# Kernel optimization log

Measured on AMD Instinct MI355X. Metric: run time of the kernel, lower is better.

## Reference

```python
import jax, jax.numpy as jnp
import numpy as np

N_NODES = 40000
N_EDGES = 640000
D_IN = 128
D_OUT = 128


def setup_inputs() -> dict:
    key = jax.random.key(0)
    k1, k2, k3, k4, k5 = jax.random.split(key, 5)
    x = jax.random.normal(k1, (N_NODES, D_IN), dtype=jnp.float32)
    row = jax.random.randint(k2, (N_EDGES,), 0, N_NODES)
    col = jax.random.randint(k3, (N_EDGES,), 0, N_NODES)
    edge_index = jnp.stack([row, col], axis=0).astype(jnp.int64)
    # match torch uniform(-1/sqrt(in), 1/sqrt(in)) init scale
    bound = 1.0 / np.sqrt(D_IN)
    weight = jax.random.uniform(k4, (D_IN, D_OUT), minval=-bound, maxval=bound, dtype=jnp.float32)
    bias = jax.random.uniform(k5, (D_OUT,), minval=-bound, maxval=bound, dtype=jnp.float32)
    return {"x": x, "edge_index": edge_index, "weight": weight, "bias": bias}


def reference(x, edge_index, weight, bias):
    row, col = edge_index[0], edge_index[1]
    out = jnp.matmul(x, weight) + bias            # [N, D_OUT]
    out = jax.nn.relu(out)
    gathered = out[col]                            # [E, D_OUT] edge-wise gather
    agg = jax.ops.segment_max(gathered, row, num_segments=x.shape[0])  # [N, D_OUT]
    # torch_scatter scatter_max fills empty segments with 0; relu output >= 0,
    # so clamping -inf (jax empty-segment fill) to 0 reproduces that exactly.
    agg = jnp.maximum(agg, 0.0)
    return agg
```

## Files before the change

### kernel.cpp

```cpp
#include <hip/hip_runtime.h>

#define D 128
#define PADK 136
#define CAP 64
#define MAX_OVF 4096

typedef __attribute__((ext_vector_type(8))) short short8;
typedef __attribute__((ext_vector_type(4))) float floatx4;

static __device__ __forceinline__ unsigned short f2b(float f) {
    union { float f; unsigned int u; } v; v.f = f;
    return (unsigned short)((v.u + 0x7FFFu + ((v.u >> 16) & 1u)) >> 16);
}

static __device__ __forceinline__ unsigned long long pack4(
    unsigned short a, unsigned short b, unsigned short c, unsigned short d) {
    return (unsigned long long)a | ((unsigned long long)b << 16) |
           ((unsigned long long)c << 32) | ((unsigned long long)d << 48);
}

__global__ __launch_bounds__(256) void gemm_scatter_kernel(
    const float* __restrict__ x, const float* __restrict__ W,
    const float* __restrict__ bias, unsigned short* __restrict__ h, int M,
    const int* __restrict__ rows, const int* __restrict__ cols,
    int* __restrict__ cnt, int* __restrict__ cols_buf,
    int* __restrict__ ovf_cnt, int* __restrict__ ovf, int E, int GB)
{
    if ((int)blockIdx.x >= GB) {
        int e = ((int)blockIdx.x - GB) * 256 + (int)threadIdx.x;
        if (e < E) {
            int r = rows[e], c = cols[e];
            int pos = atomicAdd(&cnt[r], 1);
            if (pos < CAP) {
                cols_buf[(size_t)r * CAP + pos] = c;
            } else {
                int op = atomicAdd(ovf_cnt, 1);
                if (op < MAX_OVF) { ovf[op * 2] = r; ovf[op * 2 + 1] = c; }
            }
        }
        return;
    }

    __shared__ unsigned short Wt[D * PADK];
    __shared__ unsigned short Xs[64 * PADK];

    const int tid = threadIdx.x;

    for (int q = tid; q < D * D / 4; q += 256) {
        int n = q & (D - 1), k0 = (q >> 7) * 4;
        *(unsigned long long*)(&Wt[n * PADK + k0]) =
            pack4(f2b(W[(size_t)(k0 + 0) * D + n]), f2b(W[(size_t)(k0 + 1) * D + n]),
                  f2b(W[(size_t)(k0 + 2) * D + n]), f2b(W[(size_t)(k0 + 3) * D + n]));
    }
    const int r0 = (int)blockIdx.x * 64;
    for (int q = tid; q < 64 * D / 4; q += 256) {
        int r = q >> 5, k0 = (q & 31) * 4;
        if (r0 + r < M) {
            float4 x4 = *(const float4*)(x + (size_t)(r0 + r) * D + k0);
            *(unsigned long long*)(&Xs[r * PADK + k0]) =
                pack4(f2b(x4.x), f2b(x4.y), f2b(x4.z), f2b(x4.w));
        }
    }
    __syncthreads();

    const int wave = tid >> 6, lane = tid & 63;
    const int rw = wave * 16, mrow = lane & 15, quad = lane >> 4;

    short8 a[4];
    #pragma unroll
    for (int kc = 0; kc < 4; ++kc)
        a[kc] = *(const short8*)(&Xs[(rw + mrow) * PADK + kc * 32 + quad * 8]);

    #pragma unroll
    for (int t = 0; t < 8; ++t) {
        const int n0 = t * 16;
        floatx4 acc = {0.f, 0.f, 0.f, 0.f};
        #pragma unroll
        for (int kc = 0; kc < 4; ++kc) {
            short8 b = *(const short8*)(&Wt[(n0 + mrow) * PADK + kc * 32 + quad * 8]);
            acc = __builtin_amdgcn_mfma_f32_16x16x32_bf16(a[kc], b, acc, 0, 0, 0);
        }
        const int col = n0 + mrow;
        const float bv = bias[col];
        #pragma unroll
        for (int r = 0; r < 4; ++r) {
            int row = r0 + rw + quad * 4 + r;
            if (row < M)
                h[(size_t)row * D + col] = f2b(fmaxf(acc[r] + bv, 0.0f));
        }
    }
}

__global__ __launch_bounds__(256) void aggregate_kernel(
    const int* __restrict__ cnt, const int* __restrict__ cols_buf,
    const int* __restrict__ ovf_cnt, const int* __restrict__ ovf,
    const unsigned int* __restrict__ h2, float* __restrict__ out, int N)
{
    const int node = (int)blockIdx.x * 4 + ((int)threadIdx.x >> 6);
    if (node >= N) return;
    const int lane = threadIdx.x & 63;
    const int* mycols = cols_buf + (size_t)node * CAP;
    const int end = min(cnt[node], CAP);
    float2 acc = make_float2(0.0f, 0.0f);
    int i = 0;
    for (; i + 7 < end; i += 8) {
        unsigned int v[8];
        #pragma unroll
        for (int u = 0; u < 8; ++u)
            v[u] = h2[(size_t)mycols[i + u] * 64 + lane];
        #pragma unroll
        for (int u = 0; u < 8; ++u) {
            acc.x = fmaxf(acc.x, __uint_as_float(v[u] << 16));
            acc.y = fmaxf(acc.y, __uint_as_float(v[u] & 0xFFFF0000u));
        }
    }
    for (; i < end; ++i) {
        unsigned int v = h2[(size_t)mycols[i] * 64 + lane];
        acc.x = fmaxf(acc.x, __uint_as_float(v << 16));
        acc.y = fmaxf(acc.y, __uint_as_float(v & 0xFFFF0000u));
    }
    const int oc = min(*ovf_cnt, MAX_OVF);
    for (int k = 0; k < oc; ++k) {
        if (ovf[k * 2] == node) {
            unsigned int v = h2[(size_t)ovf[k * 2 + 1] * 64 + lane];
            acc.x = fmaxf(acc.x, __uint_as_float(v << 16));
            acc.y = fmaxf(acc.y, __uint_as_float(v & 0xFFFF0000u));
        }
    }
    ((float2*)out)[(size_t)node * 64 + lane] = acc;
}

extern "C" void kernel_launch(void* const* d_in, const int* in_sizes, int n_in,
                              void* d_out, int out_size, void* d_ws, size_t ws_size,
                              hipStream_t stream) {
    const float* x    = (const float*)d_in[0];
    const int*   ei   = (const int*)d_in[1];
    const float* W    = (const float*)d_in[2];
    const float* bias = (const float*)d_in[3];

    const int N = in_sizes[0] / D;
    const int E = in_sizes[1] / 2;
    const int* rows = ei;
    const int* cols = ei + E;

    char* ws = (char*)d_ws;
    size_t off_h    = 0;
    size_t off_cnt  = off_h   + (size_t)N * D * sizeof(unsigned short);
    size_t off_ovfc = off_cnt + (size_t)N * sizeof(int);
    size_t off_ovf  = off_ovfc + 4 * sizeof(int);
    size_t off_cb   = off_ovf + (size_t)MAX_OVF * 2 * sizeof(int);

    unsigned short* h = (unsigned short*)(ws + off_h);
    int* cnt          = (int*)(ws + off_cnt);
    int* ovf_cnt      = (int*)(ws + off_ovfc);
    int* ovf          = (int*)(ws + off_ovf);
    int* cols_buf     = (int*)(ws + off_cb);

    hipMemsetAsync(cnt, 0, (size_t)(N + 4) * sizeof(int), stream);

    const int GB = (N + 63) / 64;
    const int SB = (E + 255) / 256;
    gemm_scatter_kernel<<<GB + SB, 256, 0, stream>>>(
        x, W, bias, h, N, rows, cols, cnt, cols_buf, ovf_cnt, ovf, E, GB);

    aggregate_kernel<<<(N + 3) / 4, 256, 0, stream>>>(
        cnt, cols_buf, ovf_cnt, ovf, (const unsigned int*)h, (float*)d_out, N);
}
```

Measured before the change: 154.3 us.

## Partition edge scatter by XCD so atomics on each row stay in one L2

The edge-bucketing blocks become a grid-stride loop in which each block only handles edges whose row index maps to its own XCD (bid mod 8). This keeps the atomics on cnt[r] and the cols_buf writes for a given row inside one XCD's L2, avoiding cross-die coherence traffic. The cost is that every XCD group reads the full row array, so row reads happen eight times over. The W load into shared memory is also changed to coalesced float4 reads with a transposed scalar store, and the GEMM block count is padded to a multiple of 8 with an early exit for the padding blocks.

```diff
diff --git a/kernel.cpp b/kernel.cpp
--- a/kernel.cpp
+++ b/kernel.cpp
@@ -4,6 +4,7 @@
 #define PADK 136
 #define CAP 64
 #define MAX_OVF 4096
+#define NXCD 8
 
 typedef __attribute__((ext_vector_type(8))) short short8;
 typedef __attribute__((ext_vector_type(4))) float floatx4;
@@ -24,35 +25,47 @@
     const float* __restrict__ bias, unsigned short* __restrict__ h, int M,
     const int* __restrict__ rows, const int* __restrict__ cols,
     int* __restrict__ cnt, int* __restrict__ cols_buf,
-    int* __restrict__ ovf_cnt, int* __restrict__ ovf, int E, int GB)
+    int* __restrict__ ovf_cnt, int* __restrict__ ovf, int E, int GB, int SBG)
 {
-    if ((int)blockIdx.x >= GB) {
-        int e = ((int)blockIdx.x - GB) * 256 + (int)threadIdx.x;
-        if (e < E) {
-            int r = rows[e], c = cols[e];
-            int pos = atomicAdd(&cnt[r], 1);
-            if (pos < CAP) {
-                cols_buf[(size_t)r * CAP + pos] = c;
-            } else {
-                int op = atomicAdd(ovf_cnt, 1);
-                if (op < MAX_OVF) { ovf[op * 2] = r; ovf[op * 2 + 1] = c; }
+    const int bid = (int)blockIdx.x;
+    if (bid >= GB) {
+        const int xcd  = bid & (NXCD - 1);
+        const int rank = (bid - GB) >> 3;
+        for (int e0 = rank * 256; e0 < E; e0 += SBG * 256) {
+            int e = e0 + (int)threadIdx.x;
+            if (e < E) {
+                int r = rows[e];
+                if ((r & (NXCD - 1)) == xcd) {
+                    int c = cols[e];
+                    int pos = atomicAdd(&cnt[r], 1);
+                    if (pos < CAP) {
+                        cols_buf[(size_t)r * CAP + pos] = c;
+                    } else {
+                        int op = atomicAdd(ovf_cnt, 1);
+                        if (op < MAX_OVF) { ovf[op * 2] = r; ovf[op * 2 + 1] = c; }
+                    }
+                }
             }
         }
         return;
     }
+
+    const int r0 = bid * 64;
+    if (r0 >= M) return;
 
     __shared__ unsigned short Wt[D * PADK];
     __shared__ unsigned short Xs[64 * PADK];
 
     const int tid = threadIdx.x;
 
-    for (int q = tid; q < D * D / 4; q += 256) {
-        int n = q & (D - 1), k0 = (q >> 7) * 4;
-        *(unsigned long long*)(&Wt[n * PADK + k0]) =
-            pack4(f2b(W[(size_t)(k0 + 0) * D + n]), f2b(W[(size_t)(k0 + 1) * D + n]),
-                  f2b(W[(size_t)(k0 + 2) * D + n]), f2b(W[(size_t)(k0 + 3) * D + n]));
+    for (int idx = tid * 4; idx < D * D; idx += 1024) {
+        float4 w4 = *(const float4*)(W + idx);
+        int k = idx >> 7, n = idx & (D - 1);
+        Wt[(n + 0) * PADK + k] = f2b(w4.x);
+        Wt[(n + 1) * PADK + k] = f2b(w4.y);
+        Wt[(n + 2) * PADK + k] = f2b(w4.z);
+        Wt[(n + 3) * PADK + k] = f2b(w4.w);
     }
-    const int r0 = (int)blockIdx.x * 64;
     for (int q = tid; q < 64 * D / 4; q += 256) {
         int r = q >> 5, k0 = (q & 31) * 4;
         if (r0 + r < M) {
@@ -158,10 +171,12 @@
 
     hipMemsetAsync(cnt, 0, (size_t)(N + 4) * sizeof(int), stream);
 
-    const int GB = (N + 63) / 64;
-    const int SB = (E + 255) / 256;
+    int GB = (N + 63) / 64;
+    GB = (GB + 7) & ~7;
+    const int SBG = 256;
+    const int SB  = SBG * NXCD;
     gemm_scatter_kernel<<<GB + SB, 256, 0, stream>>>(
-        x, W, bias, h, N, rows, cols, cnt, cols_buf, ovf_cnt, ovf, E, GB);
+        x, W, bias, h, N, rows, cols, cnt, cols_buf, ovf_cnt, ovf, E, GB, SBG);
 
     aggregate_kernel<<<(N + 3) / 4, 256, 0, stream>>>(
         cnt, cols_buf, ovf_cnt, ovf, (const unsigned int*)h, (float*)d_out, N);
```

Result: faster. 150.5 us (-2.4%).

## Precompute bf16 weight once, XCD-partition scatter atomics, keep W tiles in registers

Applied to the files above, without the earlier changes.

A new prep kernel zeroes the counters with vector stores, replacing the memset, and converts W to transposed bf16 once in workspace. Each GEMM block then loads its two 16-column W slices straight into registers instead of every block rebuilding the full W tile in LDS. The scatter blocks are reorganised so that each XCD-indexed block handles only rows whose low bits match its XCD, aiming to keep atomics on cnt local to one L2. This adds an extra kernel launch, and the scatter blocks now read the row array eight times.

```diff
diff --git a/kernel.cpp b/kernel.cpp
--- a/kernel.cpp
+++ b/kernel.cpp
@@ -4,6 +4,7 @@
 #define PADK 136
 #define CAP 64
 #define MAX_OVF 4096
+#define NXCD 8
 
 typedef __attribute__((ext_vector_type(8))) short short8;
 typedef __attribute__((ext_vector_type(4))) float floatx4;
@@ -19,40 +20,85 @@
            ((unsigned long long)c << 32) | ((unsigned long long)d << 48);
 }
 
+__global__ __launch_bounds__(256) void prep_kernel(
+    const float* __restrict__ W, unsigned short* __restrict__ Wt_g,
+    int* __restrict__ cnt, int nzero)
+{
+    const int bid = (int)blockIdx.x, tid = threadIdx.x;
+    if (bid < 40) {
+        int i4 = bid * 256 + tid;
+        if (i4 * 4 < nzero) ((int4*)cnt)[i4] = make_int4(0, 0, 0, 0);
+        return;
+    }
+    int q = (bid - 40) * 256 + tid;
+    int n = q & (D - 1), k0 = (q >> 7) * 4;
+    *(unsigned long long*)(Wt_g + (size_t)n * D + k0) =
+        pack4(f2b(W[(size_t)(k0 + 0) * D + n]), f2b(W[(size_t)(k0 + 1) * D + n]),
+              f2b(W[(size_t)(k0 + 2) * D + n]), f2b(W[(size_t)(k0 + 3) * D + n]));
+}
+
 __global__ __launch_bounds__(256) void gemm_scatter_kernel(
-    const float* __restrict__ x, const float* __restrict__ W,
+    const float* __restrict__ x, const unsigned short* __restrict__ Wt_g,
     const float* __restrict__ bias, unsigned short* __restrict__ h, int M,
     const int* __restrict__ rows, const int* __restrict__ cols,
     int* __restrict__ cnt, int* __restrict__ cols_buf,
     int* __restrict__ ovf_cnt, int* __restrict__ ovf, int E, int GB)
 {
-    if ((int)blockIdx.x >= GB) {
-        int e = ((int)blockIdx.x - GB) * 256 + (int)threadIdx.x;
-        if (e < E) {
-            int r = rows[e], c = cols[e];
-            int pos = atomicAdd(&cnt[r], 1);
-            if (pos < CAP) {
-                cols_buf[(size_t)r * CAP + pos] = c;
-            } else {
-                int op = atomicAdd(ovf_cnt, 1);
-                if (op < MAX_OVF) { ovf[op * 2] = r; ovf[op * 2 + 1] = c; }
+    const int bid = (int)blockIdx.x;
+    const int tid = threadIdx.x;
+
+    if (bid >= GB) {
+        const int xcd   = bid & (NXCD - 1);
+        const int chunk = (bid - GB) >> 3;
+        const int e0 = chunk * 1024 + tid;
+        int r[4], c[4], pos[4];
+        bool v[4];
+        #pragma unroll
+        for (int i = 0; i < 4; ++i) {
+            int e = e0 + i * 256;
+            v[i] = false;
+            if (e < E) {
+                r[i] = rows[e];
+                v[i] = ((r[i] & (NXCD - 1)) == xcd);
+                if (v[i]) c[i] = cols[e];
             }
         }
+        #pragma unroll
+        for (int i = 0; i < 4; ++i)
+            if (v[i]) pos[i] = atomicAdd(&cnt[r[i]], 1);
+        #pragma unroll
+        for (int i = 0; i < 4; ++i) {
+            if (v[i]) {
+                if (pos[i] < CAP) {
+                    cols_buf[(size_t)r[i] * CAP + pos[i]] = c[i];
+                } else {
+                    int op = atomicAdd(ovf_cnt, 1);
+                    if (op < MAX_OVF) { ovf[op * 2] = r[i]; ovf[op * 2 + 1] = c[i]; }
+                }
+            }
+        }
         return;
     }
 
-    __shared__ unsigned short Wt[D * PADK];
+    const int r0 = bid * 64;
+    if (r0 >= M) return;
+
     __shared__ unsigned short Xs[64 * PADK];
 
-    const int tid = threadIdx.x;
-
-    for (int q = tid; q < D * D / 4; q += 256) {
-        int n = q & (D - 1), k0 = (q >> 7) * 4;
-        *(unsigned long long*)(&Wt[n * PADK + k0]) =
-            pack4(f2b(W[(size_t)(k0 + 0) * D + n]), f2b(W[(size_t)(k0 + 1) * D + n]),
-                  f2b(W[(size_t)(k0 + 2) * D + n]), f2b(W[(size_t)(k0 + 3) * D + n]));
-    }
-    const int r0 = (int)blockIdx.x * 64;
+    const int wave = tid >> 6, lane = tid & 63;
+    const int mrow = lane & 15, quad = lane >> 4;
+
+    short8 breg[2][4];
+    float bv[2];
+    #pragma unroll
+    for (int t2 = 0; t2 < 2; ++t2) {
+        const int col = wave * 32 + t2 * 16 + mrow;
+        bv[t2] = bias[col];
+        #pragma unroll
+        for (int kc = 0; kc < 4; ++kc)
+            breg[t2][kc] = *(const short8*)(Wt_g + (size_t)col * D + kc * 32 + quad * 8);
+    }
+
     for (int q = tid; q < 64 * D / 4; q += 256) {
         int r = q >> 5, k0 = (q & 31) * 4;
         if (r0 + r < M) {
@@ -63,30 +109,25 @@
     }
     __syncthreads();
 
-    const int wave = tid >> 6, lane = tid & 63;
-    const int rw = wave * 16, mrow = lane & 15, quad = lane >> 4;
-
-    short8 a[4];
     #pragma unroll
-    for (int kc = 0; kc < 4; ++kc)
-        a[kc] = *(const short8*)(&Xs[(rw + mrow) * PADK + kc * 32 + quad * 8]);
-
-    #pragma unroll
-    for (int t = 0; t < 8; ++t) {
-        const int n0 = t * 16;
-        floatx4 acc = {0.f, 0.f, 0.f, 0.f};
-        #pragma unroll
-        for (int kc = 0; kc < 4; ++kc) {
-            short8 b = *(const short8*)(&Wt[(n0 + mrow) * PADK + kc * 32 + quad * 8]);
-            acc = __builtin_amdgcn_mfma_f32_16x16x32_bf16(a[kc], b, acc, 0, 0, 0);
-        }
-        const int col = n0 + mrow;
-        const float bv = bias[col];
-        #pragma unroll
-        for (int r = 0; r < 4; ++r) {
-            int row = r0 + rw + quad * 4 + r;
-            if (row < M)
-                h[(size_t)row * D + col] = f2b(fmaxf(acc[r] + bv, 0.0f));
+    for (int chunk = 0; chunk < 4; ++chunk) {
+        short8 a[4];
+        #pragma unroll
+        for (int kc = 0; kc < 4; ++kc)
+            a[kc] = *(const short8*)(&Xs[(chunk * 16 + mrow) * PADK + kc * 32 + quad * 8]);
+        #pragma unroll
+        for (int t2 = 0; t2 < 2; ++t2) {
+            floatx4 acc = {0.f, 0.f, 0.f, 0.f};
+            #pragma unroll
+            for (int kc = 0; kc < 4; ++kc)
+                acc = __builtin_amdgcn_mfma_f32_16x16x32_bf16(a[kc], breg[t2][kc], acc, 0, 0, 0);
+            const int col = wave * 32 + t2 * 16 + mrow;
+            #pragma unroll
+            for (int r = 0; r < 4; ++r) {
+                int row = r0 + chunk * 16 + quad * 4 + r;
+                if (row < M)
+                    h[(size_t)row * D + col] = f2b(fmaxf(acc[r] + bv[t2], 0.0f));
+            }
         }
     }
 }
@@ -145,23 +186,27 @@
 
     char* ws = (char*)d_ws;
     size_t off_h    = 0;
-    size_t off_cnt  = off_h   + (size_t)N * D * sizeof(unsigned short);
-    size_t off_ovfc = off_cnt + (size_t)N * sizeof(int);
+    size_t off_cnt  = off_h    + (size_t)N * D * sizeof(unsigned short);
+    size_t off_ovfc = off_cnt  + (size_t)N * sizeof(int);
     size_t off_ovf  = off_ovfc + 4 * sizeof(int);
-    size_t off_cb   = off_ovf + (size_t)MAX_OVF * 2 * sizeof(int);
-
-    unsigned short* h = (unsigned short*)(ws + off_h);
-    int* cnt          = (int*)(ws + off_cnt);
-    int* ovf_cnt      = (int*)(ws + off_ovfc);
-    int* ovf          = (int*)(ws + off_ovf);
-    int* cols_buf     = (int*)(ws + off_cb);
-
-    hipMemsetAsync(cnt, 0, (size_t)(N + 4) * sizeof(int), stream);
-
-    const int GB = (N + 63) / 64;
-    const int SB = (E + 255) / 256;
+    size_t off_wt   = off_ovf  + (size_t)MAX_OVF * 2 * sizeof(int);
+    size_t off_cb   = off_wt   + (size_t)D * D * sizeof(unsigned short);
+
+    unsigned short* h    = (unsigned short*)(ws + off_h);
+    int* cnt             = (int*)(ws + off_cnt);
+    int* ovf_cnt         = (int*)(ws + off_ovfc);
+    int* ovf             = (int*)(ws + off_ovf);
+    unsigned short* Wt_g = (unsigned short*)(ws + off_wt);
+    int* cols_buf        = (int*)(ws + off_cb);
+
+    prep_kernel<<<56, 256, 0, stream>>>(W, Wt_g, cnt, N + 4);
+
+    int GB = (N + 63) / 64;
+    GB = (GB + 7) & ~7;
+    const int NCH = (E + 1023) / 1024;
+    const int SB  = NCH * NXCD;
     gemm_scatter_kernel<<<GB + SB, 256, 0, stream>>>(
-        x, W, bias, h, N, rows, cols, cnt, cols_buf, ovf_cnt, ovf, E, GB);
+        x, Wt_g, bias, h, N, rows, cols, cnt, cols_buf, ovf_cnt, ovf, E, GB);
 
     aggregate_kernel<<<(N + 3) / 4, 256, 0, stream>>>(
         cnt, cols_buf, ovf_cnt, ovf, (const unsigned int*)h, (float*)d_out, N);
```

New measurement: 138.0 us. -10.5%, faster.
